# Optimization experiments

Measured on AMD Instinct MI355X. Metric: run time of the kernel, lower is better.

Reference implementation:

```python
import jax, jax.numpy as jnp
import numpy as np

PAD = 0.0  # self.pad fill value for padded output timesteps


def setup_inputs() -> dict:
    key = jax.random.key(0)
    ks = jax.random.split(key, 12)
    B, ST, TT, H, E, V, O = 64, 1024, 256, 512, 512, 32, 31
    s = 1.0 / np.sqrt(H)
    return {
        "trg_inputs": jax.random.randint(ks[0], (B, TT), 0, V),
        "trg_len": jax.random.randint(ks[1], (B,), 1, TT + 1),
        "source_len": jax.random.randint(ks[2], (B,), 1, ST + 1),
        "encoder_outputs": jax.random.normal(ks[3], (B, ST, H), jnp.float32),
        "encoder_last_hidden": jax.random.normal(ks[4], (1, B, H), jnp.float32),
        "embed": jax.random.normal(ks[5], (V, E), jnp.float32) * 0.02,
        "W_ih": jax.random.uniform(ks[6], (3 * H, E), jnp.float32, -s, s),
        "W_hh": jax.random.uniform(ks[7], (3 * H, H), jnp.float32, -s, s),
        "b_ih": jax.random.uniform(ks[8], (3 * H,), jnp.float32, -s, s),
        "b_hh": jax.random.uniform(ks[9], (3 * H,), jnp.float32, -s, s),
        "fc_W": jax.random.uniform(ks[10], (O, 2 * H), jnp.float32, -s, s),
        "fc_b": jax.random.uniform(ks[11], (O,), jnp.float32, -s, s),
    }


def reference(trg_inputs, trg_len, source_len, encoder_outputs,
              encoder_last_hidden, embed, W_ih, W_hh, b_ih, b_hh, fc_W, fc_b):
    B, TT = trg_inputs.shape
    ST = encoder_outputs.shape[1]
    # source-length mask replaces the per-sample truncation enc[:, :source_len]
    src_mask = jnp.arange(ST)[None, :] < source_len[:, None]  # (B, ST)
    emb = embed[trg_inputs]                 # (B, TT, E)
    xs = jnp.swapaxes(emb, 0, 1)            # (TT, B, E)
    h0 = encoder_last_hidden[0]             # (B, H), num_layers == 1

    def step(h, x):
        # PyTorch GRU cell
        gi = x @ W_ih.T + b_ih              # (B, 3H)
        gh = h @ W_hh.T + b_hh              # (B, 3H)
        i_r, i_z, i_n = jnp.split(gi, 3, axis=-1)
        h_r, h_z, h_n = jnp.split(gh, 3, axis=-1)
        r = jax.nn.sigmoid(i_r + h_r)
        z = jax.nn.sigmoid(i_z + h_z)
        n = jnp.tanh(i_n + r * h_n)
        h_new = (1.0 - z) * n + z * h       # (B, H)
        # dot attention over (masked) encoder outputs
        scores = jnp.einsum('bsh,bh->bs', encoder_outputs, h_new)
        scores = jnp.where(src_mask, scores, -1e9)
        w = jax.nn.softmax(scores, axis=-1)                 # (B, ST)
        ctx = jnp.einsum('bs,bsh->bh', w, encoder_outputs)  # (B, H)
        out = jnp.concatenate([h_new, ctx], axis=-1) @ fc_W.T + fc_b
        return h_new, out

    _, outs = jax.lax.scan(step, h0, xs)    # (TT, B, O)
    outs = jnp.swapaxes(outs, 0, 1)         # (B, TT, O)
    # timesteps >= trg_len keep the pad fill value
    t_mask = (jnp.arange(TT)[None, :] < trg_len[:, None])[:, :, None]
    return jnp.where(t_mask, outs, PAD)
```

## Files before the change

kernel.cpp:

```cpp
#include <hip/hip_runtime.h>
#include <hip/hip_bf16.h>
#include <math.h>

#define B_   64
#define ST_  1024
#define TT_  256
#define H_   512
#define E_   512
#define V_   32
#define O_   31
#define G3_  1536

__global__ __launch_bounds__(256) void k_giv(const float* __restrict__ embed,
                                             const float* __restrict__ W_ih,
                                             const float* __restrict__ b_ih,
                                             float* __restrict__ giV) {
    int idx = blockIdx.x * 256 + threadIdx.x;
    if (idx >= V_ * G3_) return;
    int v = idx / G3_, n = idx % G3_;
    const float4* e4 = (const float4*)(embed + v * E_);
    const float4* w4 = (const float4*)(W_ih + (size_t)n * E_);
    float acc = 0.f;
#pragma unroll 4
    for (int k = 0; k < E_ / 4; ++k) {
        float4 a = e4[k], b = w4[k];
        acc += a.x * b.x + a.y * b.y + a.z * b.z + a.w * b.w;
    }
    giV[idx] = acc + b_ih[n];
}

__global__ __launch_bounds__(256) void k_fcw_t(const float* __restrict__ fc_W,
                                               float* __restrict__ fc_Wt) {
    int idx = blockIdx.x * 256 + threadIdx.x;
    int k = idx >> 5, o = idx & 31;
    fc_Wt[idx] = (o < O_) ? fc_W[(size_t)o * 1024 + k] : 0.f;
}

__global__ __launch_bounds__(256) void k_gru_step(const float* __restrict__ h_prev,
                                                  int hp_stride,
                                                  const float* __restrict__ giV,
                                                  const int* __restrict__ trg,
                                                  const float* __restrict__ W_hh,
                                                  const float* __restrict__ b_hh,
                                                  float* __restrict__ h_all,
                                                  int t) {
    __shared__ float hs[8][520];
    int tid = threadIdx.x;
    int jc = blockIdx.x & 63, bc = blockIdx.x >> 6;
    int b0 = bc * 8;

#pragma unroll
    for (int i = 0; i < 4; ++i) {
        int fi = tid + i * 256;
        int bl = fi >> 7, k4 = fi & 127;
        float4 v = *(const float4*)(h_prev + (size_t)(b0 + bl) * hp_stride + k4 * 4);
        *(float4*)&hs[bl][k4 * 4] = v;
    }
    __syncthreads();

    int bl = tid & 7;
    int ks = (tid >> 3) & 3;
    int jl = tid >> 5;
    int j  = jc * 8 + jl;
    int k0 = ks * 128;

    const float4* w0 = (const float4*)(W_hh + (size_t)(j         ) * H_ + k0);
    const float4* w1 = (const float4*)(W_hh + (size_t)(j +   H_  ) * H_ + k0);
    const float4* w2 = (const float4*)(W_hh + (size_t)(j + 2 * H_) * H_ + k0);
    const float4* h4 = (const float4*)&hs[bl][k0];

    float sr = 0.f, sz = 0.f, sn = 0.f;
#pragma unroll 8
    for (int k = 0; k < 32; ++k) {
        float4 hv = h4[k];
        float4 a = w0[k], c = w1[k], d = w2[k];
        sr += hv.x * a.x + hv.y * a.y + hv.z * a.z + hv.w * a.w;
        sz += hv.x * c.x + hv.y * c.y + hv.z * c.z + hv.w * c.w;
        sn += hv.x * d.x + hv.y * d.y + hv.z * d.z + hv.w * d.w;
    }
    sr += __shfl_xor(sr, 8);  sr += __shfl_xor(sr, 16);
    sz += __shfl_xor(sz, 8);  sz += __shfl_xor(sz, 16);
    sn += __shfl_xor(sn, 8);  sn += __shfl_xor(sn, 16);

    if (ks == 0) {
        int b = b0 + bl;
        int tok = trg[(size_t)b * TT_ + t];
        const float* gv = giV + (size_t)tok * G3_;
        float gh_r = sr + b_hh[j];
        float gh_z = sz + b_hh[H_ + j];
        float gh_n = sn + b_hh[2 * H_ + j];
        float r = 1.f / (1.f + expf(-(gv[j] + gh_r)));
        float z = 1.f / (1.f + expf(-(gv[H_ + j] + gh_z)));
        float n = tanhf(gv[2 * H_ + j] + r * gh_n);
        float hp = hs[bl][j];
        h_all[(size_t)b * TT_ * H_ + (size_t)t * H_ + j] = (1.f - z) * n + z * hp;
    }
}

#define FMA16(a, bb)                                                     \
    acc[0][0] = fmaf(a.x, bb.x, acc[0][0]);                              \
    acc[0][1] = fmaf(a.x, bb.y, acc[0][1]);                              \
    acc[0][2] = fmaf(a.x, bb.z, acc[0][2]);                              \
    acc[0][3] = fmaf(a.x, bb.w, acc[0][3]);                              \
    acc[1][0] = fmaf(a.y, bb.x, acc[1][0]);                              \
    acc[1][1] = fmaf(a.y, bb.y, acc[1][1]);                              \
    acc[1][2] = fmaf(a.y, bb.z, acc[1][2]);                              \
    acc[1][3] = fmaf(a.y, bb.w, acc[1][3]);                              \
    acc[2][0] = fmaf(a.z, bb.x, acc[2][0]);                              \
    acc[2][1] = fmaf(a.z, bb.y, acc[2][1]);                              \
    acc[2][2] = fmaf(a.z, bb.z, acc[2][2]);                              \
    acc[2][3] = fmaf(a.z, bb.w, acc[2][3]);                              \
    acc[3][0] = fmaf(a.w, bb.x, acc[3][0]);                              \
    acc[3][1] = fmaf(a.w, bb.y, acc[3][1]);                              \
    acc[3][2] = fmaf(a.w, bb.z, acc[3][2]);                              \
    acc[3][3] = fmaf(a.w, bb.w, acc[3][3]);

__global__ __launch_bounds__(256) void k_scores(const float* __restrict__ h_all,
                                                const float* __restrict__ enc,
                                                float* __restrict__ wgt) {
    __shared__ float As[16][68];
    __shared__ float Bs[16][68];
    int b  = blockIdx.z;
    int m0 = blockIdx.y * 64, n0 = blockIdx.x * 64;
    int tid = threadIdx.x;
    int tx = tid & 15, ty = tid >> 4;
    int lr = tid >> 2, lk = (tid & 3) * 4;

    const float* Abase = h_all + (size_t)b * TT_ * H_ + (size_t)(m0 + lr) * H_ + lk;
    const float* Bbase = enc   + (size_t)b * ST_ * H_ + (size_t)(n0 + lr) * H_ + lk;

    float acc[4][4] = {};
    for (int k0 = 0; k0 < H_; k0 += 16) {
        float4 av = *(const float4*)(Abase + k0);
        float4 bv = *(const float4*)(Bbase + k0);
        __syncthreads();
        As[lk + 0][lr] = av.x; As[lk + 1][lr] = av.y;
        As[lk + 2][lr] = av.z; As[lk + 3][lr] = av.w;
        Bs[lk + 0][lr] = bv.x; Bs[lk + 1][lr] = bv.y;
        Bs[lk + 2][lr] = bv.z; Bs[lk + 3][lr] = bv.w;
        __syncthreads();
#pragma unroll
        for (int kk = 0; kk < 16; ++kk) {
            float4 a  = *(const float4*)&As[kk][ty * 4];
            float4 bb = *(const float4*)&Bs[kk][tx * 4];
            FMA16(a, bb)
        }
    }
#pragma unroll
    for (int i = 0; i < 4; ++i)
#pragma unroll
        for (int jj = 0; jj < 4; ++jj)
            wgt[(size_t)b * TT_ * ST_ + (size_t)(m0 + ty * 4 + i) * ST_ + (n0 + tx * 4 + jj)] = acc[i][jj];
}

__global__ __launch_bounds__(256) void k_softmax(float* __restrict__ wgt,
                                                 const int* __restrict__ source_len) {
    __shared__ float red[8];
    int row = blockIdx.x;
    int b = row >> 8;
    int slen = source_len[b];
    float* W = wgt + (size_t)row * ST_;
    int tid = threadIdx.x;

    float v[4];
    float mx = -3.0e38f;
#pragma unroll
    for (int i = 0; i < 4; ++i) {
        int s = tid + i * 256;
        v[i] = (s < slen) ? W[s] : -1e9f;
        mx = fmaxf(mx, v[i]);
    }
#pragma unroll
    for (int off = 32; off; off >>= 1) mx = fmaxf(mx, __shfl_xor(mx, off));
    int wv = tid >> 6;
    if ((tid & 63) == 0) red[wv] = mx;
    __syncthreads();
    mx = fmaxf(fmaxf(red[0], red[1]), fmaxf(red[2], red[3]));

    float sm = 0.f;
#pragma unroll
    for (int i = 0; i < 4; ++i) {
        v[i] = expf(v[i] - mx);
        sm += v[i];
    }
#pragma unroll
    for (int off = 32; off; off >>= 1) sm += __shfl_xor(sm, off);
    if ((tid & 63) == 0) red[4 + wv] = sm;
    __syncthreads();
    sm = red[4] + red[5] + red[6] + red[7];
    float inv = 1.f / sm;
#pragma unroll
    for (int i = 0; i < 4; ++i)
        W[tid + i * 256] = v[i] * inv;
}

__global__ __launch_bounds__(256) void k_ctx(const float* __restrict__ wgt,
                                             const float* __restrict__ enc,
                                             float* __restrict__ ctx) {
    __shared__ float As[16][68];
    __shared__ float Bs[16][68];
    int b  = blockIdx.z;
    int m0 = blockIdx.y * 64, n0 = blockIdx.x * 64;
    int tid = threadIdx.x;
    int tx = tid & 15, ty = tid >> 4;
    int lr = tid >> 2, lk = (tid & 3) * 4;
    int bk = tid >> 4, bn = (tid & 15) * 4;

    const float* Abase = wgt + (size_t)b * TT_ * ST_ + (size_t)(m0 + lr) * ST_ + lk;
    const float* Bbase = enc + (size_t)b * ST_ * H_ + n0 + bn;

    float acc[4][4] = {};
    for (int k0 = 0; k0 < ST_; k0 += 16) {
        float4 av = *(const float4*)(Abase + k0);
        float4 bv = *(const float4*)(Bbase + (size_t)(k0 + bk) * H_);
        __syncthreads();
        As[lk + 0][lr] = av.x; As[lk + 1][lr] = av.y;
        As[lk + 2][lr] = av.z; As[lk + 3][lr] = av.w;
        *(float4*)&Bs[bk][bn] = bv;
        __syncthreads();
#pragma unroll
        for (int kk = 0; kk < 16; ++kk) {
            float4 a  = *(const float4*)&As[kk][ty * 4];
            float4 bb = *(const float4*)&Bs[kk][tx * 4];
            FMA16(a, bb)
        }
    }
#pragma unroll
    for (int i = 0; i < 4; ++i)
#pragma unroll
        for (int jj = 0; jj < 4; ++jj)
            ctx[(size_t)b * TT_ * H_ + (size_t)(m0 + ty * 4 + i) * H_ + (n0 + tx * 4 + jj)] = acc[i][jj];
}

__global__ __launch_bounds__(256) void k_out(const float* __restrict__ h_all,
                                             const float* __restrict__ ctx,
                                             const float* __restrict__ fc_Wt,
                                             const float* __restrict__ fc_b,
                                             const int* __restrict__ trg_len,
                                             float* __restrict__ out) {
    int tid = threadIdx.x;
    int o = tid & 31;
    int m = blockIdx.x * 8 + (tid >> 5);
    int b = m >> 8, t = m & 255;
    const float* xh = h_all + (size_t)m * H_;
    const float* xc = ctx + (size_t)m * H_;
    float acc = (o < O_) ? fc_b[o] : 0.f;
#pragma unroll 4
    for (int k = 0; k < H_; ++k) acc = fmaf(xh[k], fc_Wt[k * 32 + o], acc);
#pragma unroll 4
    for (int k = 0; k < H_; ++k) acc = fmaf(xc[k], fc_Wt[(H_ + k) * 32 + o], acc);
    if (o < O_) {
        float val = (t < trg_len[b]) ? acc : 0.0f;
        out[(size_t)m * O_ + o] = val;
    }
}

extern "C" void kernel_launch(void* const* d_in, const int* in_sizes, int n_in,
                              void* d_out, int out_size, void* d_ws, size_t ws_size,
                              hipStream_t stream) {
    const int*   trg      = (const int*)d_in[0];
    const int*   trg_len  = (const int*)d_in[1];
    const int*   src_len  = (const int*)d_in[2];
    const float* enc      = (const float*)d_in[3];
    const float* enc_last = (const float*)d_in[4];
    const float* embed    = (const float*)d_in[5];
    const float* W_ih     = (const float*)d_in[6];
    const float* W_hh     = (const float*)d_in[7];
    const float* b_ih     = (const float*)d_in[8];
    const float* b_hh     = (const float*)d_in[9];
    const float* fc_W     = (const float*)d_in[10];
    const float* fc_b     = (const float*)d_in[11];
    float* out = (float*)d_out;

    char* ws = (char*)d_ws;
    float* giV   = (float*)ws;  ws += (size_t)V_ * G3_ * 4;
    float* fc_Wt = (float*)ws;  ws += (size_t)1024 * 32 * 4;
    float* h_all = (float*)ws;  ws += (size_t)B_ * TT_ * H_ * 4;
    float* wgt   = (float*)ws;  ws += (size_t)B_ * TT_ * ST_ * 4;
    float* ctx   = (float*)ws;  ws += (size_t)B_ * TT_ * H_ * 4;

    k_giv<<<192, 256, 0, stream>>>(embed, W_ih, b_ih, giV);
    k_fcw_t<<<128, 256, 0, stream>>>(fc_W, fc_Wt);

    for (int t = 0; t < TT_; ++t) {
        const float* hp = t ? (h_all + (size_t)(t - 1) * H_) : enc_last;
        int stride = t ? TT_ * H_ : H_;
        k_gru_step<<<512, 256, 0, stream>>>(hp, stride, giV, trg, W_hh, b_hh, h_all, t);
    }

    k_scores<<<dim3(ST_ / 64, TT_ / 64, B_), 256, 0, stream>>>(h_all, enc, wgt);
    k_softmax<<<B_ * TT_, 256, 0, stream>>>(wgt, src_len);
    k_ctx<<<dim3(H_ / 64, TT_ / 64, B_), 256, 0, stream>>>(wgt, enc, ctx);
    k_out<<<B_ * TT_ / 8, 256, 0, stream>>>(h_all, ctx, fc_Wt, fc_b, trg_len, out);
}
```

Measured before the change: 3.256 ms.

## Fuse per-timestep GRU launches into one persistent kernel with grid barrier

Replaces the 256 per-timestep GRU kernel launches with a single persistent kernel of 512 blocks. The blocks synchronise between timesteps through a two-level atomic barrier (32 leaf counters feeding one root counter), and hidden state is read and written with agent-scope atomics. The aim is to remove per-launch overhead and launch gaps on the serial recurrence. It relies on all 512 blocks being co-resident, which launch_bounds(256,2) is meant to help with; if they are not, the kernel deadlocks. It also adds spin-wait cost at every step.

Result: slower. 4.755 ms (+46.0%).

```diff
diff --git a/kernel.cpp b/kernel.cpp
--- a/kernel.cpp
+++ b/kernel.cpp
@@ -36,27 +36,17 @@
     fc_Wt[idx] = (o < O_) ? fc_W[(size_t)o * 1024 + k] : 0.f;
 }
 
-__global__ __launch_bounds__(256) void k_gru_step(const float* __restrict__ h_prev,
-                                                  int hp_stride,
-                                                  const float* __restrict__ giV,
-                                                  const int* __restrict__ trg,
-                                                  const float* __restrict__ W_hh,
-                                                  const float* __restrict__ b_hh,
-                                                  float* __restrict__ h_all,
-                                                  int t) {
+__global__ __launch_bounds__(256, 2) void k_gru_all(const float* __restrict__ enc_last,
+                                                    const float* __restrict__ giV,
+                                                    const int* __restrict__ trg,
+                                                    const float* __restrict__ W_hh,
+                                                    const float* __restrict__ b_hh,
+                                                    float* __restrict__ h_all,
+                                                    unsigned* __restrict__ bar) {
     __shared__ float hs[8][520];
     int tid = threadIdx.x;
     int jc = blockIdx.x & 63, bc = blockIdx.x >> 6;
     int b0 = bc * 8;
-
-#pragma unroll
-    for (int i = 0; i < 4; ++i) {
-        int fi = tid + i * 256;
-        int bl = fi >> 7, k4 = fi & 127;
-        float4 v = *(const float4*)(h_prev + (size_t)(b0 + bl) * hp_stride + k4 * 4);
-        *(float4*)&hs[bl][k4 * 4] = v;
-    }
-    __syncthreads();
 
     int bl = tid & 7;
     int ks = (tid >> 3) & 3;
@@ -68,32 +58,69 @@
     const float4* w1 = (const float4*)(W_hh + (size_t)(j +   H_  ) * H_ + k0);
     const float4* w2 = (const float4*)(W_hh + (size_t)(j + 2 * H_) * H_ + k0);
     const float4* h4 = (const float4*)&hs[bl][k0];
-
-    float sr = 0.f, sz = 0.f, sn = 0.f;
+    float bh_r = b_hh[j], bh_z = b_hh[H_ + j], bh_n = b_hh[2 * H_ + j];
+
+    unsigned* leaf = bar + (size_t)(blockIdx.x & 31) * 16;
+    unsigned* root = bar + 32 * 16;
+
+    for (int t = 0; t < TT_; ++t) {
+        const float* hbase = (t == 0) ? enc_last : (h_all + (size_t)(t - 1) * H_);
+        size_t rstride = (t == 0) ? (size_t)H_ : (size_t)TT_ * H_;
+#pragma unroll
+        for (int i = 0; i < 8; ++i) {
+            int fi = tid + i * 256;
+            int rb = fi >> 8, k2 = fi & 255;
+            const unsigned long long* p =
+                (const unsigned long long*)(hbase + (size_t)(b0 + rb) * rstride) + k2;
+            unsigned long long v = __hip_atomic_load(p, __ATOMIC_RELAXED,
+                                                     __HIP_MEMORY_SCOPE_AGENT);
+            *(unsigned long long*)&hs[rb][k2 * 2] = v;
+        }
+        __syncthreads();
+
+        float sr = 0.f, sz = 0.f, sn = 0.f;
 #pragma unroll 8
-    for (int k = 0; k < 32; ++k) {
-        float4 hv = h4[k];
-        float4 a = w0[k], c = w1[k], d = w2[k];
-        sr += hv.x * a.x + hv.y * a.y + hv.z * a.z + hv.w * a.w;
-        sz += hv.x * c.x + hv.y * c.y + hv.z * c.z + hv.w * c.w;
-        sn += hv.x * d.x + hv.y * d.y + hv.z * d.z + hv.w * d.w;
-    }
-    sr += __shfl_xor(sr, 8);  sr += __shfl_xor(sr, 16);
-    sz += __shfl_xor(sz, 8);  sz += __shfl_xor(sz, 16);
-    sn += __shfl_xor(sn, 8);  sn += __shfl_xor(sn, 16);
-
-    if (ks == 0) {
-        int b = b0 + bl;
-        int tok = trg[(size_t)b * TT_ + t];
-        const float* gv = giV + (size_t)tok * G3_;
-        float gh_r = sr + b_hh[j];
-        float gh_z = sz + b_hh[H_ + j];
-        float gh_n = sn + b_hh[2 * H_ + j];
-        float r = 1.f / (1.f + expf(-(gv[j] + gh_r)));
-        float z = 1.f / (1.f + expf(-(gv[H_ + j] + gh_z)));
-        float n = tanhf(gv[2 * H_ + j] + r * gh_n);
-        float hp = hs[bl][j];
-        h_all[(size_t)b * TT_ * H_ + (size_t)t * H_ + j] = (1.f - z) * n + z * hp;
+        for (int k = 0; k < 32; ++k) {
+            float4 hv = h4[k];
+            float4 a = w0[k], c = w1[k], d = w2[k];
+            sr += hv.x * a.x + hv.y * a.y + hv.z * a.z + hv.w * a.w;
+            sz += hv.x * c.x + hv.y * c.y + hv.z * c.z + hv.w * c.w;
+            sn += hv.x * d.x + hv.y * d.y + hv.z * d.z + hv.w * d.w;
+        }
+        sr += __shfl_xor(sr, 8);  sr += __shfl_xor(sr, 16);
+        sz += __shfl_xor(sz, 8);  sz += __shfl_xor(sz, 16);
+        sn += __shfl_xor(sn, 8);  sn += __shfl_xor(sn, 16);
+
+        if (ks == 0) {
+            int b = b0 + bl;
+            int tok = trg[(size_t)b * TT_ + t];
+            const float* gv = giV + (size_t)tok * G3_;
+            float r = 1.f / (1.f + expf(-(gv[j] + sr + bh_r)));
+            float z = 1.f / (1.f + expf(-(gv[H_ + j] + sz + bh_z)));
+            float n = tanhf(gv[2 * H_ + j] + r * (sn + bh_n));
+            float hp = hs[bl][j];
+            float hv = (1.f - z) * n + z * hp;
+            __hip_atomic_store(h_all + ((size_t)b * TT_ + t) * H_ + j, hv,
+                               __ATOMIC_RELAXED, __HIP_MEMORY_SCOPE_AGENT);
+        }
+
+        __syncthreads();
+        if (t + 1 < TT_) {
+            if (tid == 0) {
+                __builtin_amdgcn_fence(__ATOMIC_RELEASE, "agent");
+                unsigned prev = __hip_atomic_fetch_add(leaf, 1u, __ATOMIC_RELAXED,
+                                                       __HIP_MEMORY_SCOPE_AGENT);
+                if (prev == 16u * (unsigned)(t + 1) - 1u)
+                    __hip_atomic_fetch_add(root, 1u, __ATOMIC_RELAXED,
+                                           __HIP_MEMORY_SCOPE_AGENT);
+                unsigned target = 32u * (unsigned)(t + 1);
+                while (__hip_atomic_load(root, __ATOMIC_RELAXED,
+                                         __HIP_MEMORY_SCOPE_AGENT) < target)
+                    __builtin_amdgcn_s_sleep(8);
+                asm volatile("" ::: "memory");
+            }
+            __syncthreads();
+        }
     }
 }
 
@@ -273,20 +300,18 @@
     float* out = (float*)d_out;
 
     char* ws = (char*)d_ws;
-    float* giV   = (float*)ws;  ws += (size_t)V_ * G3_ * 4;
-    float* fc_Wt = (float*)ws;  ws += (size_t)1024 * 32 * 4;
-    float* h_all = (float*)ws;  ws += (size_t)B_ * TT_ * H_ * 4;
-    float* wgt   = (float*)ws;  ws += (size_t)B_ * TT_ * ST_ * 4;
-    float* ctx   = (float*)ws;  ws += (size_t)B_ * TT_ * H_ * 4;
-
+    float*    giV   = (float*)ws;    ws += (size_t)V_ * G3_ * 4;
+    float*    fc_Wt = (float*)ws;    ws += (size_t)1024 * 32 * 4;
+    float*    h_all = (float*)ws;    ws += (size_t)B_ * TT_ * H_ * 4;
+    float*    wgt   = (float*)ws;    ws += (size_t)B_ * TT_ * ST_ * 4;
+    float*    ctx   = (float*)ws;    ws += (size_t)B_ * TT_ * H_ * 4;
+    unsigned* bar   = (unsigned*)ws; ws += 4096;
+
+    hipMemsetAsync(bar, 0, 4096, stream);
     k_giv<<<192, 256, 0, stream>>>(embed, W_ih, b_ih, giV);
     k_fcw_t<<<128, 256, 0, stream>>>(fc_W, fc_Wt);
 
-    for (int t = 0; t < TT_; ++t) {
-        const float* hp = t ? (h_all + (size_t)(t - 1) * H_) : enc_last;
-        int stride = t ? TT_ * H_ : H_;
-        k_gru_step<<<512, 256, 0, stream>>>(hp, stride, giV, trg, W_hh, b_hh, h_all, t);
-    }
+    k_gru_all<<<512, 256, 0, stream>>>(enc_last, giV, trg, W_hh, b_hh, h_all, bar);
 
     k_scores<<<dim3(ST_ / 64, TT_ / 64, B_), 256, 0, stream>>>(h_all, enc, wgt);
     k_softmax<<<B_ * TT_, 256, 0, stream>>>(wgt, src_len);
```
